# Kernel tuning notes

Hardware: AMD Instinct MI355X
Metric: run time of the kernel (lower is better)

## Reference

```python
import jax, jax.numpy as jnp
import numpy as np

EPS = 1e-5
C = 6          # channels (attention length)
H = 2          # heads

def _ln(x, w, b):
    mu = jnp.mean(x, axis=-1, keepdims=True)
    var = jnp.var(x, axis=-1, keepdims=True)
    return (x - mu) * jax.lax.rsqrt(var + EPS) * w + b

def setup_inputs() -> dict:
    B, N, D = 8, 4096, 768
    S = D // C           # slot_dim = 128
    key = jax.random.key(0)
    ks = jax.random.split(key, 16)
    std = 1.0 / np.sqrt(S)
    return {
        "x": jax.random.normal(ks[0], (B, N, D), jnp.float32),
        "norm1_w": jnp.ones((D,), jnp.float32),
        "norm1_b": jnp.zeros((D,), jnp.float32),
        "norm2_w": jnp.ones((S,), jnp.float32),
        "norm2_b": jnp.zeros((S,), jnp.float32),
        "qw": jax.random.normal(ks[1], (S, S), jnp.float32) * std,
        "qb": jnp.zeros((S,), jnp.float32),
        "kw": jax.random.normal(ks[2], (S, S), jnp.float32) * std,
        "kb": jnp.zeros((S,), jnp.float32),
        "vw": jax.random.normal(ks[3], (S, S), jnp.float32) * std,
        "vb": jnp.zeros((S,), jnp.float32),
        "ow": jax.random.normal(ks[4], (S, S), jnp.float32) * std,
        "ob": jnp.zeros((S,), jnp.float32),
        "ff1w": jax.random.normal(ks[5], (S, 4 * S), jnp.float32) * std,
        "ff1b": jnp.zeros((4 * S,), jnp.float32),
        "ff2w": jax.random.normal(ks[6], (4 * S, S), jnp.float32) * (std / 2),
        "ff2b": jnp.zeros((S,), jnp.float32),
    }

def reference(x, norm1_w, norm1_b, norm2_w, norm2_b,
              qw, qb, kw, kb, vw, vb, ow, ob,
              ff1w, ff1b, ff2w, ff2b):
    B, N, D = x.shape
    S = D // C
    hd = S // H
    scale = hd ** -0.5

    residual = x
    xn = _ln(x, norm1_w, norm1_b)                       # (B,N,D)
    xf = xn.reshape(B * N, C, S)                        # (M,C,S)
    xf = _ln(xf, norm2_w, norm2_b)

    # MHA over C=6 channel tokens per (B*N) slot
    M = B * N
    q = (xf @ qw + qb).reshape(M, C, H, hd)
    k = (xf @ kw + kb).reshape(M, C, H, hd)
    v = (xf @ vw + vb).reshape(M, C, H, hd)
    attn = jnp.einsum('mqhd,mkhd->mhqk', q, k) * scale  # (M,H,C,C)
    attn = jax.nn.softmax(attn, axis=-1)
    o = jnp.einsum('mhqk,mkhd->mqhd', attn, v).reshape(M, C, S)
    att_out = o @ ow + ob

    xf = xf + att_out
    ff_in = xf
    h = _ln(xf, norm2_w, norm2_b)                       # same norm2 params reused
    h = jax.nn.gelu(h @ ff1w + ff1b, approximate=False) @ ff2w + ff2b
    xf = ff_in + h

    return residual + xf.reshape(B, N, D)
```

## Files before the change

### kernel.cpp

```cpp
#include <hip/hip_runtime.h>
#include <hip/hip_bf16.h>

typedef unsigned short u16;
typedef unsigned int u32;
using bf16x8 = __attribute__((ext_vector_type(8))) short;
using f32x4  = __attribute__((ext_vector_type(4))) float;

#define LDA   136
#define SLOTS 8
#define NROWS 48

__device__ __forceinline__ u32 pk2bf(float a, float b) {
  u32 r;
  asm("v_cvt_pk_bf16_f32 %0, %1, %2" : "=v"(r) : "v"(a), "v"(b));
  return r;
}
__device__ __forceinline__ u16 f2bf(float f) { return (u16)pk2bf(f, f); }
__device__ __forceinline__ float bf2f(u16 h) {
  union { u32 u; float f; } v; v.u = ((u32)h) << 16;
  return v.f;
}
__device__ __forceinline__ float2 bf2x2(u32 u) {
  union { u32 u; float f; } a, b; a.u = u << 16; b.u = u & 0xffff0000u;
  return make_float2(a.f, b.f);
}

#if __has_builtin(__builtin_amdgcn_exp2f)
#define EXP2F(x) __builtin_amdgcn_exp2f(x)
#else
#define EXP2F(x) exp2f(x)
#endif

#define MFMA32(a, b, c) __builtin_amdgcn_mfma_f32_16x16x32_bf16(a, b, c, 0, 0, 0)

__device__ __forceinline__ float gelu_f(float x) {
  const float a = x * x;
  const float b = fmaf(-0.10294538f, a, -2.3022077f);
  const float e = EXP2F(x * b);
  return x * __builtin_amdgcn_rcpf(1.f + e);
}

__device__ __forceinline__ void handoff() {
  __builtin_amdgcn_sched_barrier(0x7F);
  asm volatile("s_waitcnt lgkmcnt(0)" ::: "memory");
  __builtin_amdgcn_sched_barrier(0x7F);
}

__global__ void convert_w(const float* __restrict__ qw, const float* __restrict__ kw,
                          const float* __restrict__ vw, const float* __restrict__ ow,
                          const float* __restrict__ f1, const float* __restrict__ f2,
                          u16* __restrict__ o) {
  int i = blockIdx.x * 256 + threadIdx.x;
  if (i < 65536) {
    int which = i >> 14;
    const float* W = which == 0 ? qw : which == 1 ? kw : which == 2 ? vw : ow;
    int t = i & 16383;
    int n = t >> 7, k = t & 127;
    o[i] = f2bf(W[k * 128 + n]);
  } else if (i < 131072) {
    int t = i - 65536;
    int n = t >> 7, k = t & 127;
    o[i] = f2bf(f1[k * 512 + n]);
  } else if (i < 196608) {
    int t = i - 131072;
    int n = t >> 9, k = t & 511;
    o[i] = f2bf(f2[k * 128 + n]);
  }
}

__device__ __forceinline__ void gemm48T(const u16* __restrict__ A, const u16* __restrict__ WT,
                                        int ldw, f32x4 acc[3][2],
                                        int wave, int lane16, int kgrp) {
#pragma unroll
  for (int ks = 0; ks < 4; ++ks) {
    const int kk = ks * 32 + kgrp * 8;
    bf16x8 a0 = *(const bf16x8*)(A + (0 * 16 + lane16) * LDA + kk);
    bf16x8 a1 = *(const bf16x8*)(A + (1 * 16 + lane16) * LDA + kk);
    bf16x8 a2 = *(const bf16x8*)(A + (2 * 16 + lane16) * LDA + kk);
    bf16x8 b0 = *(const bf16x8*)(WT + ((wave)     * 16 + lane16) * ldw + kk);
    bf16x8 b1 = *(const bf16x8*)(WT + ((wave + 4) * 16 + lane16) * ldw + kk);
    __builtin_amdgcn_s_setprio(1);
    acc[0][0] = MFMA32(b0, a0, acc[0][0]);
    acc[1][0] = MFMA32(b0, a1, acc[1][0]);
    acc[2][0] = MFMA32(b0, a2, acc[2][0]);
    acc[0][1] = MFMA32(b1, a0, acc[0][1]);
    acc[1][1] = MFMA32(b1, a1, acc[1][1]);
    acc[2][1] = MFMA32(b1, a2, acc[2][1]);
    __builtin_amdgcn_s_setprio(0);
  }
}

__device__ __forceinline__ void store48T(u16* __restrict__ dst, f32x4 acc[3][2],
                                         const float* __restrict__ bias,
                                         int wave, int lane16, int kgrp) {
#pragma unroll
  for (int c = 0; c < 2; ++c) {
    const int col0 = (wave + 4 * c) * 16 + kgrp * 4;
    const float4 bv = *(const float4*)(bias + col0);
#pragma unroll
    for (int xr = 0; xr < 3; ++xr) {
      uint2 o;
      o.x = pk2bf(acc[xr][c][0] + bv.x, acc[xr][c][1] + bv.y);
      o.y = pk2bf(acc[xr][c][2] + bv.z, acc[xr][c][3] + bv.w);
      *(uint2*)(dst + (xr * 16 + lane16) * LDA + col0) = o;
    }
  }
}

__global__ __launch_bounds__(256, 4) void mitra_main(
    const float* __restrict__ x,
    const float* __restrict__ nw1, const float* __restrict__ nb1,
    const float* __restrict__ nw2, const float* __restrict__ nb2,
    const float* __restrict__ qb,  const float* __restrict__ kb,
    const float* __restrict__ vb,  const float* __restrict__ ob,
    const float* __restrict__ f1b, const float* __restrict__ f2b,
    const u16* __restrict__ wt, float* __restrict__ out) {
  __shared__ u16 XF[NROWS * LDA];
  __shared__ u16 BA[NROWS * LDA];
  __shared__ u16 BB[NROWS * LDA];
  __shared__ u16 PS2[2 * 48 * 8];

  const int tid    = threadIdx.x;
  const int wave   = tid >> 6;
  const int lane   = tid & 63;
  const int lane16 = lane & 15;
  const int kgrp   = lane >> 4;
  const long slot0 = (long)blockIdx.x * SLOTS;

  {
    const int s = tid >> 5, l32 = tid & 31;
    const float* xr = x + (size_t)(slot0 + s) * 768;
    float4 v[6];
    float sm = 0.f, sq = 0.f;
#pragma unroll
    for (int i = 0; i < 6; ++i) {
      v[i] = *(const float4*)(xr + (l32 + 32 * i) * 4);
      sm += v[i].x + v[i].y + v[i].z + v[i].w;
      sq += v[i].x * v[i].x + v[i].y * v[i].y + v[i].z * v[i].z + v[i].w * v[i].w;
    }
#pragma unroll
    for (int m = 1; m < 32; m <<= 1) { sm += __shfl_xor(sm, m); sq += __shfl_xor(sq, m); }
    const float mu = sm * (1.f / 768.f);
    const float rs = rsqrtf(sq * (1.f / 768.f) - mu * mu + 1e-5f);
#pragma unroll
    for (int i = 0; i < 6; ++i) {
      const float4 w = *(const float4*)(nw1 + (l32 + 32 * i) * 4);
      const float4 b = *(const float4*)(nb1 + (l32 + 32 * i) * 4);
      v[i].x = (v[i].x - mu) * rs * w.x + b.x;
      v[i].y = (v[i].y - mu) * rs * w.y + b.y;
      v[i].z = (v[i].z - mu) * rs * w.z + b.z;
      v[i].w = (v[i].w - mu) * rs * w.w + b.w;
    }
    const float4 w2 = *(const float4*)(nw2 + l32 * 4);
    const float4 b2 = *(const float4*)(nb2 + l32 * 4);
#pragma unroll
    for (int i = 0; i < 6; ++i) {
      float s2 = v[i].x + v[i].y + v[i].z + v[i].w;
      float q2 = v[i].x * v[i].x + v[i].y * v[i].y + v[i].z * v[i].z + v[i].w * v[i].w;
#pragma unroll
      for (int m = 1; m < 32; m <<= 1) { s2 += __shfl_xor(s2, m); q2 += __shfl_xor(q2, m); }
      const float mu2 = s2 * (1.f / 128.f);
      const float rs2 = rsqrtf(q2 * (1.f / 128.f) - mu2 * mu2 + 1e-5f);
      const int row = s * 6 + i;
      uint2 o;
      o.x = pk2bf((v[i].x - mu2) * rs2 * w2.x + b2.x, (v[i].y - mu2) * rs2 * w2.y + b2.y);
      o.y = pk2bf((v[i].z - mu2) * rs2 * w2.z + b2.z, (v[i].w - mu2) * rs2 * w2.w + b2.w);
      *(uint2*)(XF + row * LDA + l32 * 4) = o;
    }
  }
  __syncthreads();

  {
    f32x4 acc[3][2] = {};
    gemm48T(XF, wt + 0, 128, acc, wave, lane16, kgrp);
    store48T(BA, acc, qb, wave, lane16, kgrp);
  }
  {
    f32x4 acc[3][2] = {};
    gemm48T(XF, wt + 16384, 128, acc, wave, lane16, kgrp);
    store48T(BB, acc, kb, wave, lane16, kgrp);
  }
  __syncthreads();

  {
#pragma unroll
    for (int jl = 0; jl < 4; ++jl) {
      const int j = wave + jl * 4;
      if (j < 14) {
        const int h = j & 1;
        const int t = j >> 1;
        const int qt = (t >= 2) + (t >= 5);
        const int kt = t - 2 * qt;
        f32x4 acc = {};
#pragma unroll
        for (int ks = 0; ks < 2; ++ks) {
          const int kk = h * 64 + ks * 32 + kgrp * 8;
          const bf16x8 kf = *(const bf16x8*)(BB + (kt * 16 + lane16) * LDA + kk);
          const bf16x8 qf = *(const bf16x8*)(BA + (qt * 16 + lane16) * LDA + kk);
          acc = MFMA32(kf, qf, acc);
        }
        const int q    = qt * 16 + lane16;
        const int klo  = 6 * ((unsigned)q / 6u);
        u16* pq = PS2 + (h * 48 + q) * 8;
#pragma unroll
        for (int r = 0; r < 4; ++r) {
          const int off = kt * 16 + kgrp * 4 + r - klo;
          if ((unsigned)off < 6u) pq[off] = f2bf(acc[r] * 0.125f);
        }
      }
    }
  }
  __syncthreads();

  {
    f32x4 acc[3][2] = {};
    gemm48T(XF, wt + 32768, 128, acc, wave, lane16, kgrp);
    store48T(BA, acc, vb, wave, lane16, kgrp);
  }
  __syncthreads();

  {
    if (lane < 24) {
      const int h  = lane / 12;
      const int q  = wave * 12 + (lane % 12);
      u16* pr = PS2 + (h * 48 + q) * 8;
      float e[6];
      float m = bf2f(pr[0]);
#pragma unroll
      for (int k = 1; k < 6; ++k) m = fmaxf(m, bf2f(pr[k]));
      float ssum = 0.f;
#pragma unroll
      for (int k = 0; k < 6; ++k) { e[k] = EXP2F((bf2f(pr[k]) - m) * 1.44269504f); ssum += e[k]; }
      const float inv = __builtin_amdgcn_rcpf(ssum);
#pragma unroll
      for (int k = 0; k < 6; ++k) pr[k] = f2bf(e[k] * inv);
    }
    handoff();

    const int dseg = lane & 15;
    const int d0   = dseg * 8;
    const int h    = dseg >> 3;
    const int rgrp = lane >> 4;
#pragma unroll
    for (int p = 0; p < 3; ++p) {
      const int rl = rgrp * 3 + p;
      const int q  = wave * 12 + rl;
      const int sl = rl / 6;
      const u16* pr = PS2 + (h * 48 + q) * 8;
      const u16* vbase = BA + (wave * 12 + sl * 6) * LDA + d0;
      float o0 = 0, o1 = 0, o2 = 0, o3 = 0, o4 = 0, o5 = 0, o6 = 0, o7 = 0;
#pragma unroll
      for (int k = 0; k < 6; ++k) {
        const uint4 v4 = *(const uint4*)(vbase + k * LDA);
        const float pw = bf2f(pr[k]);
        const float2 a = bf2x2(v4.x), b = bf2x2(v4.y);
        const float2 c = bf2x2(v4.z), d = bf2x2(v4.w);
        o0 = fmaf(pw, a.x, o0); o1 = fmaf(pw, a.y, o1);
        o2 = fmaf(pw, b.x, o2); o3 = fmaf(pw, b.y, o3);
        o4 = fmaf(pw, c.x, o4); o5 = fmaf(pw, c.y, o5);
        o6 = fmaf(pw, d.x, o6); o7 = fmaf(pw, d.y, o7);
      }
      uint4 o;
      o.x = pk2bf(o0, o1); o.y = pk2bf(o2, o3);
      o.z = pk2bf(o4, o5); o.w = pk2bf(o6, o7);
      *(uint4*)(BB + q * LDA + d0) = o;
    }
  }
  __syncthreads();

  {
    f32x4 acc[3][2] = {};
    gemm48T(BB, wt + 49152, 128, acc, wave, lane16, kgrp);
#pragma unroll
    for (int c = 0; c < 2; ++c) {
      const int col0 = (wave + 4 * c) * 16 + kgrp * 4;
      const float4 bv = *(const float4*)(ob + col0);
#pragma unroll
      for (int xr = 0; xr < 3; ++xr) {
        u16* px = XF + (xr * 16 + lane16) * LDA + col0;
        const uint2 cur = *(const uint2*)px;
        const float2 lo = bf2x2(cur.x), hi = bf2x2(cur.y);
        uint2 o;
        o.x = pk2bf(lo.x + acc[xr][c][0] + bv.x, lo.y + acc[xr][c][1] + bv.y);
        o.y = pk2bf(hi.x + acc[xr][c][2] + bv.z, hi.y + acc[xr][c][3] + bv.w);
        *(uint2*)px = o;
      }
    }
  }
  __syncthreads();

  {
    const int g = tid >> 5, l32 = tid & 31;
    const float4 w2 = *(const float4*)(nw2 + l32 * 4);
    const float4 b2 = *(const float4*)(nb2 + l32 * 4);
#pragma unroll
    for (int i = 0; i < 6; ++i) {
      const int row = g * 6 + i;
      const uint2 hv = *(const uint2*)(XF + row * LDA + l32 * 4);
      const float2 lo = bf2x2(hv.x), hi = bf2x2(hv.y);
      float s2 = lo.x + lo.y + hi.x + hi.y;
      float q2 = lo.x * lo.x + lo.y * lo.y + hi.x * hi.x + hi.y * hi.y;
#pragma unroll
      for (int m = 1; m < 32; m <<= 1) { s2 += __shfl_xor(s2, m); q2 += __shfl_xor(q2, m); }
      const float mu2 = s2 * (1.f / 128.f);
      const float rs2 = rsqrtf(q2 * (1.f / 128.f) - mu2 * mu2 + 1e-5f);
      uint2 o;
      o.x = pk2bf((lo.x - mu2) * rs2 * w2.x + b2.x, (lo.y - mu2) * rs2 * w2.y + b2.y);
      o.y = pk2bf((hi.x - mu2) * rs2 * w2.z + b2.z, (hi.y - mu2) * rs2 * w2.w + b2.w);
      *(uint2*)(BA + row * LDA + l32 * 4) = o;
    }
  }

  f32x4 acc2[3][2];
#pragma unroll
  for (int c = 0; c < 2; ++c) {
    const int col0 = (wave + 4 * c) * 16 + kgrp * 4;
#pragma unroll
    for (int xr = 0; xr < 3; ++xr) {
      const uint2 t2 = *(const uint2*)(XF + (xr * 16 + lane16) * LDA + col0);
      const float2 lo = bf2x2(t2.x), hi = bf2x2(t2.y);
      acc2[xr][c][0] = lo.x; acc2[xr][c][1] = lo.y;
      acc2[xr][c][2] = hi.x; acc2[xr][c][3] = hi.y;
    }
  }
  __syncthreads();

  {
    f32x4 g[3][2] = {};
    gemm48T(BA, wt + 65536, 128, g, wave, lane16, kgrp);
#pragma unroll
    for (int c = 0; c < 2; ++c) {
      const int col0 = (wave + 4 * c) * 16 + kgrp * 4;
      const float4 bv = *(const float4*)(f1b + col0);
#pragma unroll
      for (int xr = 0; xr < 3; ++xr) {
        uint2 o;
        o.x = pk2bf(gelu_f(g[xr][c][0] + bv.x), gelu_f(g[xr][c][1] + bv.y));
        o.y = pk2bf(gelu_f(g[xr][c][2] + bv.z), gelu_f(g[xr][c][3] + bv.w));
        *(uint2*)(BB + (xr * 16 + lane16) * LDA + col0) = o;
      }
    }
  }
  __syncthreads();
#pragma unroll
  for (int t = 1; t < 4; ++t) {
    u16* const Gprev = (t & 1) ? BB : XF;
    u16* const Gcur  = (t & 1) ? XF : BB;
    gemm48T(Gprev, wt + 131072 + (t - 1) * 128, 512, acc2, wave, lane16, kgrp);
    f32x4 g[3][2] = {};
    gemm48T(BA, wt + 65536 + t * 16384, 128, g, wave, lane16, kgrp);
#pragma unroll
    for (int c = 0; c < 2; ++c) {
      const int col0 = (wave + 4 * c) * 16 + kgrp * 4;
      const float4 bv = *(const float4*)(f1b + t * 128 + col0);
#pragma unroll
      for (int xr = 0; xr < 3; ++xr) {
        uint2 o;
        o.x = pk2bf(gelu_f(g[xr][c][0] + bv.x), gelu_f(g[xr][c][1] + bv.y));
        o.y = pk2bf(gelu_f(g[xr][c][2] + bv.z), gelu_f(g[xr][c][3] + bv.w));
        *(uint2*)(Gcur + (xr * 16 + lane16) * LDA + col0) = o;
      }
    }
    __syncthreads();
  }
  gemm48T(XF, wt + 131072 + 3 * 128, 512, acc2, wave, lane16, kgrp);

#pragma unroll
  for (int c = 0; c < 2; ++c) {
    const int col0 = (wave + 4 * c) * 16 + kgrp * 4;
    const float4 fb = *(const float4*)(f2b + col0);
#pragma unroll
    for (int xr = 0; xr < 3; ++xr) {
      const int row  = xr * 16 + lane16;
      const int slot = row / 6, ch = row % 6;
      const size_t gi = (size_t)(slot0 + slot) * 768 + ch * 128 + col0;
      const float4 xv = *(const float4*)(x + gi);
      float4 o;
      o.x = xv.x + acc2[xr][c][0] + fb.x;
      o.y = xv.y + acc2[xr][c][1] + fb.y;
      o.z = xv.z + acc2[xr][c][2] + fb.z;
      o.w = xv.w + acc2[xr][c][3] + fb.w;
      *(float4*)(out + gi) = o;
    }
  }
}

extern "C" void kernel_launch(void* const* d_in, const int* in_sizes, int n_in,
                              void* d_out, int out_size, void* d_ws, size_t ws_size,
                              hipStream_t stream) {
  const float* x   = (const float*)d_in[0];
  const float* nw1 = (const float*)d_in[1];
  const float* nb1 = (const float*)d_in[2];
  const float* nw2 = (const float*)d_in[3];
  const float* nb2 = (const float*)d_in[4];
  const float* qw  = (const float*)d_in[5];
  const float* qb  = (const float*)d_in[6];
  const float* kw  = (const float*)d_in[7];
  const float* kb  = (const float*)d_in[8];
  const float* vw  = (const float*)d_in[9];
  const float* vb  = (const float*)d_in[10];
  const float* ow  = (const float*)d_in[11];
  const float* ob  = (const float*)d_in[12];
  const float* f1w = (const float*)d_in[13];
  const float* f1b = (const float*)d_in[14];
  const float* f2w = (const float*)d_in[15];
  const float* f2b = (const float*)d_in[16];
  u16* wt = (u16*)d_ws;

  convert_w<<<768, 256, 0, stream>>>(qw, kw, vw, ow, f1w, f2w, wt);

  const int M = in_sizes[0] / 768;
  mitra_main<<<M / SLOTS, 256, 0, stream>>>(x, nw1, nb1, nw2, nb2,
                                            qb, kb, vb, ob, f1b, f2b,
                                            wt, (float*)d_out);
}
```

Measured before the change: 223.1 us.

## Split each block's work across eight waves with one column tile per wave

The fused slot-attention kernel now launches 512 threads per block instead of 256. Each wave owns a single 16-column output tile rather than two. The LayerNorm, softmax and attention-times-V stages are re-indexed so each wave handles one slot. This halves per-wave register state and raises the number of resident waves per CU to hide LDS and MFMA latency. In exchange, each A fragment loaded from LDS feeds half as many MFMAs, which increases total LDS read traffic, and barriers now synchronize more waves.

```diff
diff --git a/kernel.cpp b/kernel.cpp
--- a/kernel.cpp
+++ b/kernel.cpp
@@ -68,46 +68,39 @@
   }
 }
 
-__device__ __forceinline__ void gemm48T(const u16* __restrict__ A, const u16* __restrict__ WT,
-                                        int ldw, f32x4 acc[3][2],
-                                        int wave, int lane16, int kgrp) {
+__device__ __forceinline__ void gemm48T1(const u16* __restrict__ A, const u16* __restrict__ WT,
+                                         int ldw, f32x4 acc[3],
+                                         int wave, int lane16, int kgrp) {
 #pragma unroll
   for (int ks = 0; ks < 4; ++ks) {
     const int kk = ks * 32 + kgrp * 8;
-    bf16x8 a0 = *(const bf16x8*)(A + (0 * 16 + lane16) * LDA + kk);
-    bf16x8 a1 = *(const bf16x8*)(A + (1 * 16 + lane16) * LDA + kk);
-    bf16x8 a2 = *(const bf16x8*)(A + (2 * 16 + lane16) * LDA + kk);
-    bf16x8 b0 = *(const bf16x8*)(WT + ((wave)     * 16 + lane16) * ldw + kk);
-    bf16x8 b1 = *(const bf16x8*)(WT + ((wave + 4) * 16 + lane16) * ldw + kk);
+    const bf16x8 a0 = *(const bf16x8*)(A + (0 * 16 + lane16) * LDA + kk);
+    const bf16x8 a1 = *(const bf16x8*)(A + (1 * 16 + lane16) * LDA + kk);
+    const bf16x8 a2 = *(const bf16x8*)(A + (2 * 16 + lane16) * LDA + kk);
+    const bf16x8 b  = *(const bf16x8*)(WT + (wave * 16 + lane16) * ldw + kk);
     __builtin_amdgcn_s_setprio(1);
-    acc[0][0] = MFMA32(b0, a0, acc[0][0]);
-    acc[1][0] = MFMA32(b0, a1, acc[1][0]);
-    acc[2][0] = MFMA32(b0, a2, acc[2][0]);
-    acc[0][1] = MFMA32(b1, a0, acc[0][1]);
-    acc[1][1] = MFMA32(b1, a1, acc[1][1]);
-    acc[2][1] = MFMA32(b1, a2, acc[2][1]);
+    acc[0] = MFMA32(b, a0, acc[0]);
+    acc[1] = MFMA32(b, a1, acc[1]);
+    acc[2] = MFMA32(b, a2, acc[2]);
     __builtin_amdgcn_s_setprio(0);
   }
 }
 
-__device__ __forceinline__ void store48T(u16* __restrict__ dst, f32x4 acc[3][2],
-                                         const float* __restrict__ bias,
-                                         int wave, int lane16, int kgrp) {
-#pragma unroll
-  for (int c = 0; c < 2; ++c) {
-    const int col0 = (wave + 4 * c) * 16 + kgrp * 4;
-    const float4 bv = *(const float4*)(bias + col0);
-#pragma unroll
-    for (int xr = 0; xr < 3; ++xr) {
-      uint2 o;
-      o.x = pk2bf(acc[xr][c][0] + bv.x, acc[xr][c][1] + bv.y);
-      o.y = pk2bf(acc[xr][c][2] + bv.z, acc[xr][c][3] + bv.w);
-      *(uint2*)(dst + (xr * 16 + lane16) * LDA + col0) = o;
-    }
-  }
-}
-
-__global__ __launch_bounds__(256, 4) void mitra_main(
+__device__ __forceinline__ void store48T1(u16* __restrict__ dst, f32x4 acc[3],
+                                          const float* __restrict__ bias,
+                                          int wave, int lane16, int kgrp) {
+  const int col0 = wave * 16 + kgrp * 4;
+  const float4 bv = *(const float4*)(bias + col0);
+#pragma unroll
+  for (int xr = 0; xr < 3; ++xr) {
+    uint2 o;
+    o.x = pk2bf(acc[xr][0] + bv.x, acc[xr][1] + bv.y);
+    o.y = pk2bf(acc[xr][2] + bv.z, acc[xr][3] + bv.w);
+    *(uint2*)(dst + (xr * 16 + lane16) * LDA + col0) = o;
+  }
+}
+
+__global__ __launch_bounds__(512) void mitra_main(
     const float* __restrict__ x,
     const float* __restrict__ nw1, const float* __restrict__ nb1,
     const float* __restrict__ nw2, const float* __restrict__ nb2,
@@ -128,64 +121,65 @@
   const long slot0 = (long)blockIdx.x * SLOTS;
 
   {
-    const int s = tid >> 5, l32 = tid & 31;
+    const int s = wave;
     const float* xr = x + (size_t)(slot0 + s) * 768;
-    float4 v[6];
+    const int l32 = lane & 31;
+    float4 v[3];
     float sm = 0.f, sq = 0.f;
 #pragma unroll
-    for (int i = 0; i < 6; ++i) {
-      v[i] = *(const float4*)(xr + (l32 + 32 * i) * 4);
-      sm += v[i].x + v[i].y + v[i].z + v[i].w;
-      sq += v[i].x * v[i].x + v[i].y * v[i].y + v[i].z * v[i].z + v[i].w * v[i].w;
-    }
-#pragma unroll
-    for (int m = 1; m < 32; m <<= 1) { sm += __shfl_xor(sm, m); sq += __shfl_xor(sq, m); }
+    for (int p = 0; p < 3; ++p) {
+      v[p] = *(const float4*)(xr + (p * 64 + lane) * 4);
+      sm += v[p].x + v[p].y + v[p].z + v[p].w;
+      sq += v[p].x * v[p].x + v[p].y * v[p].y + v[p].z * v[p].z + v[p].w * v[p].w;
+    }
+#pragma unroll
+    for (int m = 1; m < 64; m <<= 1) { sm += __shfl_xor(sm, m); sq += __shfl_xor(sq, m); }
     const float mu = sm * (1.f / 768.f);
     const float rs = rsqrtf(sq * (1.f / 768.f) - mu * mu + 1e-5f);
 #pragma unroll
-    for (int i = 0; i < 6; ++i) {
-      const float4 w = *(const float4*)(nw1 + (l32 + 32 * i) * 4);
-      const float4 b = *(const float4*)(nb1 + (l32 + 32 * i) * 4);
-      v[i].x = (v[i].x - mu) * rs * w.x + b.x;
-      v[i].y = (v[i].y - mu) * rs * w.y + b.y;
-      v[i].z = (v[i].z - mu) * rs * w.z + b.z;
-      v[i].w = (v[i].w - mu) * rs * w.w + b.w;
+    for (int p = 0; p < 3; ++p) {
+      const float4 w = *(const float4*)(nw1 + (p * 64 + lane) * 4);
+      const float4 b = *(const float4*)(nb1 + (p * 64 + lane) * 4);
+      v[p].x = (v[p].x - mu) * rs * w.x + b.x;
+      v[p].y = (v[p].y - mu) * rs * w.y + b.y;
+      v[p].z = (v[p].z - mu) * rs * w.z + b.z;
+      v[p].w = (v[p].w - mu) * rs * w.w + b.w;
     }
     const float4 w2 = *(const float4*)(nw2 + l32 * 4);
     const float4 b2 = *(const float4*)(nb2 + l32 * 4);
 #pragma unroll
-    for (int i = 0; i < 6; ++i) {
-      float s2 = v[i].x + v[i].y + v[i].z + v[i].w;
-      float q2 = v[i].x * v[i].x + v[i].y * v[i].y + v[i].z * v[i].z + v[i].w * v[i].w;
+    for (int p = 0; p < 3; ++p) {
+      float s2 = v[p].x + v[p].y + v[p].z + v[p].w;
+      float q2 = v[p].x * v[p].x + v[p].y * v[p].y + v[p].z * v[p].z + v[p].w * v[p].w;
 #pragma unroll
       for (int m = 1; m < 32; m <<= 1) { s2 += __shfl_xor(s2, m); q2 += __shfl_xor(q2, m); }
       const float mu2 = s2 * (1.f / 128.f);
       const float rs2 = rsqrtf(q2 * (1.f / 128.f) - mu2 * mu2 + 1e-5f);
-      const int row = s * 6 + i;
-      uint2 o;
-      o.x = pk2bf((v[i].x - mu2) * rs2 * w2.x + b2.x, (v[i].y - mu2) * rs2 * w2.y + b2.y);
-      o.y = pk2bf((v[i].z - mu2) * rs2 * w2.z + b2.z, (v[i].w - mu2) * rs2 * w2.w + b2.w);
+      const int row = s * 6 + 2 * p + (lane >> 5);
+      uint2 o;
+      o.x = pk2bf((v[p].x - mu2) * rs2 * w2.x + b2.x, (v[p].y - mu2) * rs2 * w2.y + b2.y);
+      o.y = pk2bf((v[p].z - mu2) * rs2 * w2.z + b2.z, (v[p].w - mu2) * rs2 * w2.w + b2.w);
       *(uint2*)(XF + row * LDA + l32 * 4) = o;
     }
   }
   __syncthreads();
 
   {
-    f32x4 acc[3][2] = {};
-    gemm48T(XF, wt + 0, 128, acc, wave, lane16, kgrp);
-    store48T(BA, acc, qb, wave, lane16, kgrp);
-  }
-  {
-    f32x4 acc[3][2] = {};
-    gemm48T(XF, wt + 16384, 128, acc, wave, lane16, kgrp);
-    store48T(BB, acc, kb, wave, lane16, kgrp);
-  }
-  __syncthreads();
-
-  {
-#pragma unroll
-    for (int jl = 0; jl < 4; ++jl) {
-      const int j = wave + jl * 4;
+    f32x4 acc[3] = {};
+    gemm48T1(XF, wt + 0, 128, acc, wave, lane16, kgrp);
+    store48T1(BA, acc, qb, wave, lane16, kgrp);
+  }
+  {
+    f32x4 acc[3] = {};
+    gemm48T1(XF, wt + 16384, 128, acc, wave, lane16, kgrp);
+    store48T1(BB, acc, kb, wave, lane16, kgrp);
+  }
+  __syncthreads();
+
+  {
+#pragma unroll
+    for (int jl = 0; jl < 2; ++jl) {
+      const int j = wave + jl * 8;
       if (j < 14) {
         const int h = j & 1;
         const int t = j >> 1;
@@ -213,16 +207,16 @@
   __syncthreads();
 
   {
-    f32x4 acc[3][2] = {};
-    gemm48T(XF, wt + 32768, 128, acc, wave, lane16, kgrp);
-    store48T(BA, acc, vb, wave, lane16, kgrp);
-  }
-  __syncthreads();
-
-  {
-    if (lane < 24) {
-      const int h  = lane / 12;
-      const int q  = wave * 12 + (lane % 12);
+    f32x4 acc[3] = {};
+    gemm48T1(XF, wt + 32768, 128, acc, wave, lane16, kgrp);
+    store48T1(BA, acc, vb, wave, lane16, kgrp);
+  }
+  __syncthreads();
+
+  {
+    if (lane < 12) {
+      const int h  = lane / 6;
+      const int q  = wave * 6 + (lane % 6);
       u16* pr = PS2 + (h * 48 + q) * 8;
       float e[6];
       float m = bf2f(pr[0]);
@@ -237,54 +231,44 @@
     }
     handoff();
 
-    const int dseg = lane & 15;
-    const int d0   = dseg * 8;
-    const int h    = dseg >> 3;
-    const int rgrp = lane >> 4;
+    const int d0 = (lane & 31) * 4;
+    const int h  = d0 >> 6;
+    const int rg = lane >> 5;
 #pragma unroll
     for (int p = 0; p < 3; ++p) {
-      const int rl = rgrp * 3 + p;
-      const int q  = wave * 12 + rl;
-      const int sl = rl / 6;
+      const int rl = rg * 3 + p;
+      const int q  = wave * 6 + rl;
       const u16* pr = PS2 + (h * 48 + q) * 8;
-      const u16* vbase = BA + (wave * 12 + sl * 6) * LDA + d0;
-      float o0 = 0, o1 = 0, o2 = 0, o3 = 0, o4 = 0, o5 = 0, o6 = 0, o7 = 0;
+      const u16* vbase = BA + wave * 6 * LDA + d0;
+      float o0 = 0, o1 = 0, o2 = 0, o3 = 0;
 #pragma unroll
       for (int k = 0; k < 6; ++k) {
-        const uint4 v4 = *(const uint4*)(vbase + k * LDA);
+        const uint2 v2 = *(const uint2*)(vbase + k * LDA);
         const float pw = bf2f(pr[k]);
-        const float2 a = bf2x2(v4.x), b = bf2x2(v4.y);
-        const float2 c = bf2x2(v4.z), d = bf2x2(v4.w);
+        const float2 a = bf2x2(v2.x), b = bf2x2(v2.y);
         o0 = fmaf(pw, a.x, o0); o1 = fmaf(pw, a.y, o1);
         o2 = fmaf(pw, b.x, o2); o3 = fmaf(pw, b.y, o3);
-        o4 = fmaf(pw, c.x, o4); o5 = fmaf(pw, c.y, o5);
-        o6 = fmaf(pw, d.x, o6); o7 = fmaf(pw, d.y, o7);
       }
-      uint4 o;
-      o.x = pk2bf(o0, o1); o.y = pk2bf(o2, o3);
-      o.z = pk2bf(o4, o5); o.w = pk2bf(o6, o7);
-      *(uint4*)(BB + q * LDA + d0) = o;
-    }
-  }
-  __syncthreads();
-
-  {
-    f32x4 acc[3][2] = {};
-    gemm48T(BB, wt + 49152, 128, acc, wave, lane16, kgrp);
-#pragma unroll
-    for (int c = 0; c < 2; ++c) {
-      const int col0 = (wave + 4 * c) * 16 + kgrp * 4;
-      const float4 bv = *(const float4*)(ob + col0);
-#pragma unroll
-      for (int xr = 0; xr < 3; ++xr) {
-        u16* px = XF + (xr * 16 + lane16) * LDA + col0;
-        const uint2 cur = *(const uint2*)px;
-        const float2 lo = bf2x2(cur.x), hi = bf2x2(cur.y);
-        uint2 o;
-        o.x = pk2bf(lo.x + acc[xr][c][0] + bv.x, lo.y + acc[xr][c][1] + bv.y);
-        o.y = pk2bf(hi.x + acc[xr][c][2] + bv.z, hi.y + acc[xr][c][3] + bv.w);
-        *(uint2*)px = o;
-      }
+      uint2 o; o.x = pk2bf(o0, o1); o.y = pk2bf(o2, o3);
+      *(uint2*)(BB + q * LDA + d0) = o;
+    }
+  }
+  __syncthreads();
+
+  {
+    f32x4 acc[3] = {};
+    gemm48T1(BB, wt + 49152, 128, acc, wave, lane16, kgrp);
+    const int col0 = wave * 16 + kgrp * 4;
+    const float4 bv = *(const float4*)(ob + col0);
+#pragma unroll
+    for (int xr = 0; xr < 3; ++xr) {
+      u16* px = XF + (xr * 16 + lane16) * LDA + col0;
+      const uint2 cur = *(const uint2*)px;
+      const float2 lo = bf2x2(cur.x), hi = bf2x2(cur.y);
+      uint2 o;
+      o.x = pk2bf(lo.x + acc[xr][0] + bv.x, lo.y + acc[xr][1] + bv.y);
+      o.y = pk2bf(hi.x + acc[xr][2] + bv.z, hi.y + acc[xr][3] + bv.w);
+      *(uint2*)px = o;
     }
   }
   __syncthreads();
@@ -294,8 +278,8 @@
     const float4 w2 = *(const float4*)(nw2 + l32 * 4);
     const float4 b2 = *(const float4*)(nb2 + l32 * 4);
 #pragma unroll
-    for (int i = 0; i < 6; ++i) {
-      const int row = g * 6 + i;
+    for (int i = 0; i < 3; ++i) {
+      const int row = (g >> 1) * 6 + (g & 1) * 3 + i;
       const uint2 hv = *(const uint2*)(XF + row * LDA + l32 * 4);
       const float2 lo = bf2x2(hv.x), hi = bf2x2(hv.y);
       float s2 = lo.x + lo.y + hi.x + hi.y;
@@ -311,34 +295,30 @@
     }
   }
 
-  f32x4 acc2[3][2];
-#pragma unroll
-  for (int c = 0; c < 2; ++c) {
-    const int col0 = (wave + 4 * c) * 16 + kgrp * 4;
+  f32x4 acc2[3];
+  {
+    const int col0 = wave * 16 + kgrp * 4;
 #pragma unroll
     for (int xr = 0; xr < 3; ++xr) {
       const uint2 t2 = *(const uint2*)(XF + (xr * 16 + lane16) * LDA + col0);
       const float2 lo = bf2x2(t2.x), hi = bf2x2(t2.y);
-      acc2[xr][c][0] = lo.x; acc2[xr][c][1] = lo.y;
-      acc2[xr][c][2] = hi.x; acc2[xr][c][3] = hi.y;
-    }
-  }
-  __syncthreads();
-
-  {
-    f32x4 g[3][2] = {};
-    gemm48T(BA, wt + 65536, 128, g, wave, lane16, kgrp);
-#pragma unroll
-    for (int c = 0; c < 2; ++c) {
-      const int col0 = (wave + 4 * c) * 16 + kgrp * 4;
-      const float4 bv = *(const float4*)(f1b + col0);
-#pragma unroll
-      for (int xr = 0; xr < 3; ++xr) {
-        uint2 o;
-        o.x = pk2bf(gelu_f(g[xr][c][0] + bv.x), gelu_f(g[xr][c][1] + bv.y));
-        o.y = pk2bf(gelu_f(g[xr][c][2] + bv.z), gelu_f(g[xr][c][3] + bv.w));
-        *(uint2*)(BB + (xr * 16 + lane16) * LDA + col0) = o;
-      }
+      acc2[xr][0] = lo.x; acc2[xr][1] = lo.y;
+      acc2[xr][2] = hi.x; acc2[xr][3] = hi.y;
+    }
+  }
+  __syncthreads();
+
+  {
+    f32x4 g[3] = {};
+    gemm48T1(BA, wt + 65536, 128, g, wave, lane16, kgrp);
+    const int col0 = wave * 16 + kgrp * 4;
+    const float4 bv = *(const float4*)(f1b + col0);
+#pragma unroll
+    for (int xr = 0; xr < 3; ++xr) {
+      uint2 o;
+      o.x = pk2bf(gelu_f(g[xr][0] + bv.x), gelu_f(g[xr][1] + bv.y));
+      o.y = pk2bf(gelu_f(g[xr][2] + bv.z), gelu_f(g[xr][3] + bv.w));
+      *(uint2*)(BB + (xr * 16 + lane16) * LDA + col0) = o;
     }
   }
   __syncthreads();
@@ -346,28 +326,24 @@
   for (int t = 1; t < 4; ++t) {
     u16* const Gprev = (t & 1) ? BB : XF;
     u16* const Gcur  = (t & 1) ? XF : BB;
-    gemm48T(Gprev, wt + 131072 + (t - 1) * 128, 512, acc2, wave, lane16, kgrp);
-    f32x4 g[3][2] = {};
-    gemm48T(BA, wt + 65536 + t * 16384, 128, g, wave, lane16, kgrp);
-#pragma unroll
-    for (int c = 0; c < 2; ++c) {
-      const int col0 = (wave + 4 * c) * 16 + kgrp * 4;
-      const float4 bv = *(const float4*)(f1b + t * 128 + col0);
-#pragma unroll
-      for (int xr = 0; xr < 3; ++xr) {
-        uint2 o;
-        o.x = pk2bf(gelu_f(g[xr][c][0] + bv.x), gelu_f(g[xr][c][1] + bv.y));
-        o.y = pk2bf(gelu_f(g[xr][c][2] + bv.z), gelu_f(g[xr][c][3] + bv.w));
-        *(uint2*)(Gcur + (xr * 16 + lane16) * LDA + col0) = o;
-      }
+    gemm48T1(Gprev, wt + 131072 + (t - 1) * 128, 512, acc2, wave, lane16, kgrp);
+    f32x4 g[3] = {};
+    gemm48T1(BA, wt + 65536 + t * 16384, 128, g, wave, lane16, kgrp);
+    const int col0 = wave * 16 + kgrp * 4;
+    const float4 bv = *(const float4*)(f1b + t * 128 + col0);
+#pragma unroll
+    for (int xr = 0; xr < 3; ++xr) {
+      uint2 o;
+      o.x = pk2bf(gelu_f(g[xr][0] + bv.x), gelu_f(g[xr][1] + bv.y));
+      o.y = pk2bf(gelu_f(g[xr][2] + bv.z), gelu_f(g[xr][3] + bv.w));
+      *(uint2*)(Gcur + (xr * 16 + lane16) * LDA + col0) = o;
     }
     __syncthreads();
   }
-  gemm48T(XF, wt + 131072 + 3 * 128, 512, acc2, wave, lane16, kgrp);
-
-#pragma unroll
-  for (int c = 0; c < 2; ++c) {
-    const int col0 = (wave + 4 * c) * 16 + kgrp * 4;
+  gemm48T1(XF, wt + 131072 + 3 * 128, 512, acc2, wave, lane16, kgrp);
+
+  {
+    const int col0 = wave * 16 + kgrp * 4;
     const float4 fb = *(const float4*)(f2b + col0);
 #pragma unroll
     for (int xr = 0; xr < 3; ++xr) {
@@ -376,10 +352,10 @@
       const size_t gi = (size_t)(slot0 + slot) * 768 + ch * 128 + col0;
       const float4 xv = *(const float4*)(x + gi);
       float4 o;
-      o.x = xv.x + acc2[xr][c][0] + fb.x;
-      o.y = xv.y + acc2[xr][c][1] + fb.y;
-      o.z = xv.z + acc2[xr][c][2] + fb.z;
-      o.w = xv.w + acc2[xr][c][3] + fb.w;
+      o.x = xv.x + acc2[xr][0] + fb.x;
+      o.y = xv.y + acc2[xr][1] + fb.y;
+      o.z = xv.z + acc2[xr][2] + fb.z;
+      o.w = xv.w + acc2[xr][3] + fb.w;
       *(float4*)(out + gi) = o;
     }
   }
@@ -410,7 +386,7 @@
   convert_w<<<768, 256, 0, stream>>>(qw, kw, vw, ow, f1w, f2w, wt);
 
   const int M = in_sizes[0] / 768;
-  mitra_main<<<M / SLOTS, 256, 0, stream>>>(x, nw1, nb1, nw2, nb2,
+  mitra_main<<<M / SLOTS, 512, 0, stream>>>(x, nw1, nb1, nw2, nb2,
                                             qb, kb, vb, ob, f1b, f2b,
                                             wt, (float*)d_out);
 }
```

Result: slower. 230.5 us (+3.3%).
